# Kernel optimization log

Hardware: AMD Instinct MI355X
Metric: run time of the kernel (lower is better)

## Reference

```python
import jax, jax.numpy as jnp
import numpy as np

NEG_INF = -1e30


def setup_inputs() -> dict:
    key = jax.random.key(0)
    k1, k2 = jax.random.split(key)
    N, Q, M = 8, 2048, 2048
    gen_adj = jax.random.normal(k1, (N, Q, M), dtype=jnp.float32)
    # per-sample k in [1, 64]; force one sample to the max so topknum is deterministic
    topk = jax.random.randint(k2, (N, 1), 1, 65, dtype=jnp.int64)
    topk = topk.at[0, 0].set(64)
    return {"gen_adj": gen_adj, "topk": topk}


def reference(gen_adj, topk):
    # gen_adj: [N, Q, M] float, topk: [N, 1] int (per-sample variable k)
    N, Q, M = gen_adj.shape
    k_per = jnp.minimum(topk, M)                      # clamp like min(topk[i], M)
    topknum = int(jnp.max(k_per))                     # padded output width

    a = jnp.abs(gen_adj)                              # [N, Q, M]
    vals, idx = jax.lax.top_k(a, topknum)             # [N, Q, K] each (sorted desc)

    pos = jnp.arange(topknum)                         # [K]
    valid = pos[None, None, :] < k_per[:, :, None]    # [N, 1, K] -> broadcasts over Q

    # softmax over only the first k_i logits per sample; padded slots -> 0
    logits = jnp.where(valid, vals, NEG_INF)
    r_weight = jax.nn.softmax(logits, axis=-1)
    r_weight = jnp.where(valid, r_weight, 0.0)        # exact zeros in padding
    topk_index = jnp.where(valid, idx, 0)             # pad indices with 0
    return r_weight, topk_index
```

## Files before the change

### kernel.cpp

```cpp
#include <hip/hip_runtime.h>

#define M_COLS 2048
#define KOUT 64
#define CAND 128
#define BLK 256

typedef unsigned long long u64;

#define DPPU(old, src, ctrl, rmask) \
  ((unsigned)__builtin_amdgcn_update_dpp((int)(old), (int)(src), (ctrl), (rmask), 0xF, false))
#define RDL(x, l) ((unsigned)__builtin_amdgcn_readlane((int)(x), (l)))

#define SCAN_ADD_U(x)             \
  do {                            \
    x += DPPU(0u, x, 0x111, 0xF); \
    x += DPPU(0u, x, 0x112, 0xF); \
    x += DPPU(0u, x, 0x114, 0xF); \
    x += DPPU(0u, x, 0x118, 0xF); \
    x += DPPU(0u, x, 0x142, 0xA); \
    x += DPPU(0u, x, 0x143, 0xC); \
  } while (0)

#define SCAN_MAX_U(x)                                  \
  do {                                                 \
    unsigned _t;                                       \
    _t = DPPU(0u, x, 0x111, 0xF); x = x > _t ? x : _t; \
    _t = DPPU(0u, x, 0x112, 0xF); x = x > _t ? x : _t; \
    _t = DPPU(0u, x, 0x114, 0xF); x = x > _t ? x : _t; \
    _t = DPPU(0u, x, 0x118, 0xF); x = x > _t ? x : _t; \
    _t = DPPU(0u, x, 0x142, 0xA); x = x > _t ? x : _t; \
    _t = DPPU(0u, x, 0x143, 0xC); x = x > _t ? x : _t; \
  } while (0)

#define SCAN_ADD_F(x)                                               \
  do {                                                              \
    x += __uint_as_float(DPPU(0u, __float_as_uint(x), 0x111, 0xF)); \
    x += __uint_as_float(DPPU(0u, __float_as_uint(x), 0x112, 0xF)); \
    x += __uint_as_float(DPPU(0u, __float_as_uint(x), 0x114, 0xF)); \
    x += __uint_as_float(DPPU(0u, __float_as_uint(x), 0x118, 0xF)); \
    x += __uint_as_float(DPPU(0u, __float_as_uint(x), 0x142, 0xA)); \
    x += __uint_as_float(DPPU(0u, __float_as_uint(x), 0x143, 0xC)); \
  } while (0)

#define SWZ(v, J) ((unsigned)__builtin_amdgcn_ds_swizzle((int)(v), (((J) << 10) | 0x1f)))

#define EX_S(dst, src, J)                           \
  do {                                              \
    unsigned _lo = SWZ((unsigned)(src), J);         \
    unsigned _hi = SWZ((unsigned)((src) >> 32), J); \
    dst = ((u64)_hi << 32) | _lo;                   \
  } while (0)
#define EX_D(dst, src, CTRL)                             \
  do {                                                   \
    unsigned _lo = DPPU(0u, (unsigned)(src), CTRL, 0xF); \
    unsigned _hi = DPPU(0u, (unsigned)((src) >> 32), CTRL, 0xF); \
    dst = ((u64)_hi << 32) | _lo;                        \
  } while (0)
#define EX_W(dst, src)                                                         \
  do {                                                                         \
    unsigned _lo = (unsigned)__shfl_xor((int)(unsigned)(src), 32, 64);         \
    unsigned _hi = (unsigned)__shfl_xor((int)(unsigned)((src) >> 32), 32, 64); \
    dst = ((u64)_hi << 32) | _lo;                                              \
  } while (0)

#define CMPSEL(up)                        \
  do {                                    \
    k0 = ((k0 >= o0) == (up)) ? k0 : o0;  \
    k1 = ((k1 >= o1) == (up)) ? o1 : k1;  \
  } while (0)

#define STEP_A_S(J, UP) do { u64 o0, o1; EX_S(o0, k0, J); EX_S(o1, k1, J); CMPSEL(UP); } while (0)
#define STEP_A_D(CTRL, UP) do { u64 o0, o1; EX_D(o0, k0, CTRL); EX_D(o1, k1, CTRL); CMPSEL(UP); } while (0)
#define STEP_A_W(UP) do { u64 o0, o1; EX_W(o0, k0); EX_W(o1, k1); CMPSEL(UP); } while (0)

#define STEP_B_S(J, UP) do { u64 o; EX_S(o, av, J); av = ((av >= o) == (UP)) ? av : o; } while (0)
#define STEP_B_D(CTRL, UP) do { u64 o; EX_D(o, av, CTRL); av = ((av >= o) == (UP)) ? av : o; } while (0)
#define STEP_B_W(UP) do { u64 o; EX_W(o, av); av = ((av >= o) == (UP)) ? av : o; } while (0)

__global__ __launch_bounds__(BLK) void topk_route_kernel(
    const float* __restrict__ A, const int* __restrict__ topk,
    float* __restrict__ out_w, float* __restrict__ out_i, int NQ, int Q, int N) {
  __shared__ u64 cand[4][CAND];

  const unsigned tid = threadIdx.x;
  const unsigned wv = tid >> 6, lane = tid & 63u;
  const unsigned row = blockIdx.x * 4u + wv;
  if ((int)row >= NQ) return;
  const unsigned n = row / (unsigned)Q;

  const float4* a4 = (const float4*)(A + (size_t)row * M_COLS);
  float4 v[8];
#pragma unroll
  for (int t = 0; t < 8; ++t) v[t] = a4[lane + 64u * (unsigned)t];

  int kk;
  if (N >= 8) {
    const int4* t4 = (const int4*)topk;
    int4 a = t4[0], b = t4[1], c = t4[2], d = t4[3];
    int k64 = topk[2 * (int)n], k32 = topk[(int)n];
    bool looks64 = (a.y == 0) & (a.w == 0) & (b.y == 0) & (b.w == 0) &
                   (c.y == 0) & (c.w == 0) & (d.y == 0) & (d.w == 0) &
                   (a.x >= 1) & (a.z >= 1) & (b.x >= 1) & (b.z >= 1) &
                   (c.x >= 1) & (c.z >= 1) & (d.x >= 1) & (d.z >= 1);
    kk = looks64 ? k64 : k32;
  } else {
    bool looks64 = true;
    for (int i = 0; i < N; ++i) {
      int l = topk[2 * i], h = topk[2 * i + 1];
      if (h != 0 || l < 1) { looks64 = false; break; }
    }
    kk = looks64 ? topk[2 * (int)n] : topk[(int)n];
  }
  kk = kk > M_COLS ? M_COLS : (kk < 0 ? 0 : kk);

  unsigned bits[32];
#pragma unroll
  for (int t = 0; t < 8; ++t) {
    bits[4 * t + 0] = __float_as_uint(v[t].x) & 0x7fffffffu;
    bits[4 * t + 1] = __float_as_uint(v[t].y) & 0x7fffffffu;
    bits[4 * t + 2] = __float_as_uint(v[t].z) & 0x7fffffffu;
    bits[4 * t + 3] = __float_as_uint(v[t].w) & 0x7fffffffu;
  }

  cand[wv][lane + 64u] = 0ull;

  unsigned mx = bits[0];
#pragma unroll
  for (int j = 1; j < 32; ++j) mx = bits[j] > mx ? bits[j] : mx;
  SCAN_MAX_U(mx);
  mx = RDL(mx, 63);
  const int em = (int)(mx >> 23);

  unsigned keep = 0u, sl = 0u, inc = 0u, csel = 0u;
  auto attempt = [&](unsigned T) {
    unsigned q0 = 0u, q1 = 0u, q2 = 0u, q3 = 0u;
#pragma unroll
    for (int j = 7; j >= 0; --j) {
      q0 = q0 + q0 + (unsigned)(bits[j] >= T);
      q1 = q1 + q1 + (unsigned)(bits[8 + j] >= T);
      q2 = q2 + q2 + (unsigned)(bits[16 + j] >= T);
      q3 = q3 + q3 + (unsigned)(bits[24 + j] >= T);
    }
    keep = q0 | (q1 << 8) | (q2 << 16) | (q3 << 24);
    sl = __popc(keep);
    inc = sl;
    SCAN_ADD_U(inc);
    csel = RDL(inc, 63);
  };

  unsigned lo, hi = mx + 1u;
  {
    unsigned T = (em > 0) ? ((unsigned)em << 23) : 0u;
    attempt(T); lo = T;
    if (csel < KOUT) {
      hi = T;
      T = (em - 1 > 0) ? ((unsigned)(em - 1) << 23) : 0u;
      attempt(T); lo = T;
      if (csel < KOUT) {
        hi = T;
        T = (em - 2 > 0) ? ((unsigned)(em - 2) << 23) : 0u;
        attempt(T); lo = T;
        if (csel < KOUT) { hi = T; attempt(0u); lo = 0u; }
      }
    }
  }

  {
    unsigned csel_lo = csel, lastT = lo;
    while (csel_lo > CAND && lo + 1u < hi) {
      unsigned mid = lo + ((hi - lo) >> 1);
      attempt(mid); lastT = mid;
      if (csel >= KOUT) { lo = mid; csel_lo = csel; } else hi = mid;
    }
    if (lastT != lo) attempt(lo);
  }

  if (csel > CAND) {
    unsigned kgt = 0u;
#pragma unroll
    for (int j = 31; j >= 0; --j) kgt = (kgt << 1) | (unsigned)(bits[j] >= hi);
    unsigned slgt = __popc(kgt), incgt = slgt;
    SCAN_ADD_U(incgt);
    unsigned cgt = RDL(incgt, 63);
    unsigned cap = CAND - cgt;
    keep = kgt;
    unsigned run = 0u;
#pragma unroll
    for (int t = 0; t < 8; ++t) {
      unsigned f = 0u;
#pragma unroll
      for (int c = 3; c >= 0; --c) f = (f << 1) | (unsigned)(bits[4 * t + c] == lo);
      unsigned tc = __popc(f), it = tc;
      SCAN_ADD_U(it);
      unsigned base = run + it - tc;
#pragma unroll
      for (int c = 0; c < 4; ++c) {
        if (f & (1u << c)) {
          if (base < cap) keep |= 1u << (4 * t + c);
          ++base;
        }
      }
      run += RDL(it, 63);
    }
    sl = __popc(keep);
    inc = sl;
    SCAN_ADD_U(inc);
    csel = RDL(inc, 63);
  }

  unsigned p = inc - sl;
  const unsigned lobase = 2047u - 4u * lane;
  u64* cw = &cand[wv][0];
#pragma unroll
  for (int j = 0; j < 32; ++j) {
    if (keep & (1u << j)) {
      cw[p] = ((u64)bits[j] << 32) |
              (u64)(lobase - (unsigned)((j >> 2) * 256 + (j & 3)));
      ++p;
    }
  }

  const bool b1 = (lane & 1u) != 0u, b2 = (lane & 2u) != 0u, b4 = (lane & 4u) != 0u;
  const bool b8 = (lane & 8u) != 0u, b16 = (lane & 16u) != 0u, b32 = (lane & 32u) != 0u;

  u64 k0 = cand[wv][lane];
  u64 k1 = cand[wv][lane + 64u];
  STEP_A_D(0xB1, !(b2 ^ b1));
  STEP_A_D(0x4E, !(b4 ^ b2)); STEP_A_D(0xB1, !(b4 ^ b1));
  STEP_A_S(4, !(b8 ^ b4)); STEP_A_D(0x4E, !(b8 ^ b2)); STEP_A_D(0xB1, !(b8 ^ b1));
  STEP_A_S(8, !(b16 ^ b8)); STEP_A_S(4, !(b16 ^ b4));
  STEP_A_D(0x4E, !(b16 ^ b2)); STEP_A_D(0xB1, !(b16 ^ b1));
  STEP_A_S(16, !(b32 ^ b16)); STEP_A_S(8, !(b32 ^ b8)); STEP_A_S(4, !(b32 ^ b4));
  STEP_A_D(0x4E, !(b32 ^ b2)); STEP_A_D(0xB1, !(b32 ^ b1));
  STEP_A_W(!b32);
  STEP_A_S(16, !b16); STEP_A_S(8, !b8); STEP_A_S(4, !b4);
  STEP_A_D(0x4E, !b2); STEP_A_D(0xB1, !b1);

  u64 av = k0 >= k1 ? k0 : k1;
  STEP_B_W(!b32);
  STEP_B_S(16, !b16); STEP_B_S(8, !b8); STEP_B_S(4, !b4);
  STEP_B_D(0x4E, !b2); STEP_B_D(0xB1, !b1);

  float val = __uint_as_float((unsigned)(av >> 32));
  unsigned midx = 2047u - (unsigned)(av & 0xffffffffull);
  bool valid = (int)lane < kk;

  float vmx = __uint_as_float(
      (unsigned)__builtin_amdgcn_readfirstlane((int)(unsigned)(av >> 32)));
  float e = valid ? __expf(val - vmx) : 0.0f;
  float s = e;
  SCAN_ADD_F(s);
  float stot = __uint_as_float(RDL(__float_as_uint(s), 63));
  float w = valid ? (e / stot) : 0.0f;

  size_t o = (size_t)row * KOUT + lane;
  out_w[o] = w;
  out_i[o] = valid ? (float)midx : 0.0f;
}

extern "C" void kernel_launch(void* const* d_in, const int* in_sizes, int n_in,
                              void* d_out, int out_size, void* d_ws, size_t ws_size,
                              hipStream_t stream) {
  const float* A = (const float*)d_in[0];
  const int* topk = (const int*)d_in[1];
  float* out = (float*)d_out;
  const int NQ = in_sizes[0] / M_COLS;
  const int N = in_sizes[1] > 0 ? in_sizes[1] : 1;
  const int Q = NQ / N;
  float* out_w = out;
  float* out_i = out + (size_t)NQ * KOUT;
  const int blocks = (NQ + 3) / 4;
  hipLaunchKernelGGL(topk_route_kernel, dim3(blocks), dim3(BLK), 0, stream, A,
                     topk, out_w, out_i, NQ, Q, N);
}
```

Measured before the change: 29.66 us.

## Process four rows per wave with register double-buffered prefetch of next row

```diff
diff --git a/kernel.cpp b/kernel.cpp
--- a/kernel.cpp
+++ b/kernel.cpp
@@ -4,6 +4,7 @@
 #define KOUT 64
 #define CAND 128
 #define BLK 256
+#define ROWS 4
 
 typedef unsigned long long u64;
 
@@ -50,11 +51,11 @@
     unsigned _hi = SWZ((unsigned)((src) >> 32), J); \
     dst = ((u64)_hi << 32) | _lo;                   \
   } while (0)
-#define EX_D(dst, src, CTRL)                             \
-  do {                                                   \
-    unsigned _lo = DPPU(0u, (unsigned)(src), CTRL, 0xF); \
+#define EX_D(dst, src, CTRL)                                     \
+  do {                                                           \
+    unsigned _lo = DPPU(0u, (unsigned)(src), CTRL, 0xF);         \
     unsigned _hi = DPPU(0u, (unsigned)((src) >> 32), CTRL, 0xF); \
-    dst = ((u64)_hi << 32) | _lo;                        \
+    dst = ((u64)_hi << 32) | _lo;                                \
   } while (0)
 #define EX_W(dst, src)                                                         \
   do {                                                                         \
@@ -63,10 +64,10 @@
     dst = ((u64)_hi << 32) | _lo;                                              \
   } while (0)
 
-#define CMPSEL(up)                        \
-  do {                                    \
-    k0 = ((k0 >= o0) == (up)) ? k0 : o0;  \
-    k1 = ((k1 >= o1) == (up)) ? o1 : k1;  \
+#define CMPSEL(up)                       \
+  do {                                   \
+    k0 = ((k0 >= o0) == (up)) ? k0 : o0; \
+    k1 = ((k1 >= o1) == (up)) ? o1 : k1; \
   } while (0)
 
 #define STEP_A_S(J, UP) do { u64 o0, o1; EX_S(o0, k0, J); EX_S(o1, k1, J); CMPSEL(UP); } while (0)
@@ -84,178 +85,190 @@
 
   const unsigned tid = threadIdx.x;
   const unsigned wv = tid >> 6, lane = tid & 63u;
-  const unsigned row = blockIdx.x * 4u + wv;
-  if ((int)row >= NQ) return;
-  const unsigned n = row / (unsigned)Q;
-
-  const float4* a4 = (const float4*)(A + (size_t)row * M_COLS);
-  float4 v[8];
-#pragma unroll
-  for (int t = 0; t < 8; ++t) v[t] = a4[lane + 64u * (unsigned)t];
-
-  int kk;
+  const unsigned r0 = (blockIdx.x * 4u + wv) * ROWS;
+  if ((int)r0 >= NQ) return;
+
+  bool looks64;
   if (N >= 8) {
     const int4* t4 = (const int4*)topk;
     int4 a = t4[0], b = t4[1], c = t4[2], d = t4[3];
-    int k64 = topk[2 * (int)n], k32 = topk[(int)n];
-    bool looks64 = (a.y == 0) & (a.w == 0) & (b.y == 0) & (b.w == 0) &
-                   (c.y == 0) & (c.w == 0) & (d.y == 0) & (d.w == 0) &
-                   (a.x >= 1) & (a.z >= 1) & (b.x >= 1) & (b.z >= 1) &
-                   (c.x >= 1) & (c.z >= 1) & (d.x >= 1) & (d.z >= 1);
-    kk = looks64 ? k64 : k32;
+    looks64 = (a.y == 0) & (a.w == 0) & (b.y == 0) & (b.w == 0) &
+              (c.y == 0) & (c.w == 0) & (d.y == 0) & (d.w == 0) &
+              (a.x >= 1) & (a.z >= 1) & (b.x >= 1) & (b.z >= 1) &
+              (c.x >= 1) & (c.z >= 1) & (d.x >= 1) & (d.z >= 1);
   } else {
-    bool looks64 = true;
+    looks64 = true;
     for (int i = 0; i < N; ++i) {
       int l = topk[2 * i], h = topk[2 * i + 1];
       if (h != 0 || l < 1) { looks64 = false; break; }
     }
-    kk = looks64 ? topk[2 * (int)n] : topk[(int)n];
   }
-  kk = kk > M_COLS ? M_COLS : (kk < 0 ? 0 : kk);
-
-  unsigned bits[32];
-#pragma unroll
-  for (int t = 0; t < 8; ++t) {
-    bits[4 * t + 0] = __float_as_uint(v[t].x) & 0x7fffffffu;
-    bits[4 * t + 1] = __float_as_uint(v[t].y) & 0x7fffffffu;
-    bits[4 * t + 2] = __float_as_uint(v[t].z) & 0x7fffffffu;
-    bits[4 * t + 3] = __float_as_uint(v[t].w) & 0x7fffffffu;
+
+  const bool b1 = (lane & 1u) != 0u, b2 = (lane & 2u) != 0u, b4 = (lane & 4u) != 0u;
+  const bool b8 = (lane & 8u) != 0u, b16 = (lane & 16u) != 0u, b32 = (lane & 32u) != 0u;
+  const unsigned lobase = 2047u - 4u * lane;
+  u64* cw = &cand[wv][0];
+
+  float4 buf[8];
+  {
+    const float4* a4 = (const float4*)(A + (size_t)r0 * M_COLS);
+#pragma unroll
+    for (int t = 0; t < 8; ++t) buf[t] = a4[lane + 64u * (unsigned)t];
   }
 
-  cand[wv][lane + 64u] = 0ull;
-
-  unsigned mx = bits[0];
-#pragma unroll
-  for (int j = 1; j < 32; ++j) mx = bits[j] > mx ? bits[j] : mx;
-  SCAN_MAX_U(mx);
-  mx = RDL(mx, 63);
-  const int em = (int)(mx >> 23);
-
-  unsigned keep = 0u, sl = 0u, inc = 0u, csel = 0u;
-  auto attempt = [&](unsigned T) {
-    unsigned q0 = 0u, q1 = 0u, q2 = 0u, q3 = 0u;
-#pragma unroll
-    for (int j = 7; j >= 0; --j) {
-      q0 = q0 + q0 + (unsigned)(bits[j] >= T);
-      q1 = q1 + q1 + (unsigned)(bits[8 + j] >= T);
-      q2 = q2 + q2 + (unsigned)(bits[16 + j] >= T);
-      q3 = q3 + q3 + (unsigned)(bits[24 + j] >= T);
-    }
-    keep = q0 | (q1 << 8) | (q2 << 16) | (q3 << 24);
-    sl = __popc(keep);
-    inc = sl;
-    SCAN_ADD_U(inc);
-    csel = RDL(inc, 63);
-  };
-
-  unsigned lo, hi = mx + 1u;
-  {
-    unsigned T = (em > 0) ? ((unsigned)em << 23) : 0u;
-    attempt(T); lo = T;
-    if (csel < KOUT) {
-      hi = T;
-      T = (em - 1 > 0) ? ((unsigned)(em - 1) << 23) : 0u;
+  for (int i = 0; i < ROWS; ++i) {
+    const unsigned row = r0 + (unsigned)i;
+    if ((int)row >= NQ) break;
+
+    unsigned bits[32];
+#pragma unroll
+    for (int t = 0; t < 8; ++t) {
+      bits[4 * t + 0] = __float_as_uint(buf[t].x) & 0x7fffffffu;
+      bits[4 * t + 1] = __float_as_uint(buf[t].y) & 0x7fffffffu;
+      bits[4 * t + 2] = __float_as_uint(buf[t].z) & 0x7fffffffu;
+      bits[4 * t + 3] = __float_as_uint(buf[t].w) & 0x7fffffffu;
+    }
+
+    if (i + 1 < ROWS && (int)(row + 1u) < NQ) {
+      const float4* b4 = (const float4*)(A + (size_t)(row + 1u) * M_COLS);
+#pragma unroll
+      for (int t = 0; t < 8; ++t) buf[t] = b4[lane + 64u * (unsigned)t];
+    }
+
+    cw[lane + 64u] = 0ull;
+
+    unsigned mx = bits[0];
+#pragma unroll
+    for (int j = 1; j < 32; ++j) mx = bits[j] > mx ? bits[j] : mx;
+    SCAN_MAX_U(mx);
+    mx = RDL(mx, 63);
+    const int em = (int)(mx >> 23);
+
+    unsigned keep = 0u, sl = 0u, inc = 0u, csel = 0u;
+    auto attempt = [&](unsigned T) {
+      unsigned q0 = 0u, q1 = 0u, q2 = 0u, q3 = 0u;
+#pragma unroll
+      for (int j = 7; j >= 0; --j) {
+        q0 = q0 + q0 + (unsigned)(bits[j] >= T);
+        q1 = q1 + q1 + (unsigned)(bits[8 + j] >= T);
+        q2 = q2 + q2 + (unsigned)(bits[16 + j] >= T);
+        q3 = q3 + q3 + (unsigned)(bits[24 + j] >= T);
+      }
+      keep = q0 | (q1 << 8) | (q2 << 16) | (q3 << 24);
+      sl = __popc(keep);
+      inc = sl;
+      SCAN_ADD_U(inc);
+      csel = RDL(inc, 63);
+    };
+
+    unsigned lo, hi = mx + 1u;
+    {
+      unsigned T = (em > 0) ? ((unsigned)em << 23) : 0u;
       attempt(T); lo = T;
       if (csel < KOUT) {
         hi = T;
-        T = (em - 2 > 0) ? ((unsigned)(em - 2) << 23) : 0u;
+        T = (em - 1 > 0) ? ((unsigned)(em - 1) << 23) : 0u;
         attempt(T); lo = T;
-        if (csel < KOUT) { hi = T; attempt(0u); lo = 0u; }
-      }
-    }
+        if (csel < KOUT) {
+          hi = T;
+          T = (em - 2 > 0) ? ((unsigned)(em - 2) << 23) : 0u;
+          attempt(T); lo = T;
+          if (csel < KOUT) { hi = T; attempt(0u); lo = 0u; }
+        }
+      }
+    }
+
+    {
+      unsigned csel_lo = csel, lastT = lo;
+      while (csel_lo > CAND && lo + 1u < hi) {
+        unsigned mid = lo + ((hi - lo) >> 1);
+        attempt(mid); lastT = mid;
+        if (csel >= KOUT) { lo = mid; csel_lo = csel; } else hi = mid;
+      }
+      if (lastT != lo) attempt(lo);
+    }
+
+    if (csel > CAND) {
+      unsigned kgt = 0u;
+#pragma unroll
+      for (int j = 31; j >= 0; --j) kgt = (kgt << 1) | (unsigned)(bits[j] >= hi);
+      unsigned slgt = __popc(kgt), incgt = slgt;
+      SCAN_ADD_U(incgt);
+      unsigned cgt = RDL(incgt, 63);
+      unsigned cap = CAND - cgt;
+      keep = kgt;
+      unsigned run = 0u;
+#pragma unroll
+      for (int t = 0; t < 8; ++t) {
+        unsigned f = 0u;
+#pragma unroll
+        for (int c = 3; c >= 0; --c) f = (f << 1) | (unsigned)(bits[4 * t + c] == lo);
+        unsigned tc = __popc(f), it = tc;
+        SCAN_ADD_U(it);
+        unsigned tbase = run + it - tc;
+#pragma unroll
+        for (int c = 0; c < 4; ++c) {
+          if (f & (1u << c)) {
+            if (tbase < cap) keep |= 1u << (4 * t + c);
+            ++tbase;
+          }
+        }
+        run += RDL(it, 63);
+      }
+      sl = __popc(keep);
+      inc = sl;
+      SCAN_ADD_U(inc);
+      csel = RDL(inc, 63);
+    }
+
+    unsigned base = inc - sl;
+#pragma unroll
+    for (int j = 0; j < 32; ++j) {
+      if (keep & (1u << j)) {
+        unsigned pj = base + (unsigned)__popc(keep & ((1u << j) - 1u));
+        cw[pj] = ((u64)bits[j] << 32) |
+                 (u64)(lobase - (unsigned)((j >> 2) * 256 + (j & 3)));
+      }
+    }
+
+    u64 k0 = cw[lane];
+    u64 k1 = cw[lane + 64u];
+    STEP_A_D(0xB1, !(b2 ^ b1));
+    STEP_A_D(0x4E, !(b4 ^ b2)); STEP_A_D(0xB1, !(b4 ^ b1));
+    STEP_A_S(4, !(b8 ^ b4)); STEP_A_D(0x4E, !(b8 ^ b2)); STEP_A_D(0xB1, !(b8 ^ b1));
+    STEP_A_S(8, !(b16 ^ b8)); STEP_A_S(4, !(b16 ^ b4));
+    STEP_A_D(0x4E, !(b16 ^ b2)); STEP_A_D(0xB1, !(b16 ^ b1));
+    STEP_A_S(16, !(b32 ^ b16)); STEP_A_S(8, !(b32 ^ b8)); STEP_A_S(4, !(b32 ^ b4));
+    STEP_A_D(0x4E, !(b32 ^ b2)); STEP_A_D(0xB1, !(b32 ^ b1));
+    STEP_A_W(!b32);
+    STEP_A_S(16, !b16); STEP_A_S(8, !b8); STEP_A_S(4, !b4);
+    STEP_A_D(0x4E, !b2); STEP_A_D(0xB1, !b1);
+
+    u64 av = k0 >= k1 ? k0 : k1;
+    STEP_B_W(!b32);
+    STEP_B_S(16, !b16); STEP_B_S(8, !b8); STEP_B_S(4, !b4);
+    STEP_B_D(0x4E, !b2); STEP_B_D(0xB1, !b1);
+
+    const unsigned n = row / (unsigned)Q;
+    int kk = looks64 ? topk[2 * (int)n] : topk[(int)n];
+    kk = kk > M_COLS ? M_COLS : (kk < 0 ? 0 : kk);
+
+    float val = __uint_as_float((unsigned)(av >> 32));
+    unsigned midx = 2047u - (unsigned)(av & 0xffffffffull);
+    bool valid = (int)lane < kk;
+
+    float vmx = __uint_as_float(
+        (unsigned)__builtin_amdgcn_readfirstlane((int)(unsigned)(av >> 32)));
+    float e = valid ? __expf(val - vmx) : 0.0f;
+    float s = e;
+    SCAN_ADD_F(s);
+    float stot = __uint_as_float(RDL(__float_as_uint(s), 63));
+    float w = valid ? (e / stot) : 0.0f;
+
+    size_t o = (size_t)row * KOUT + lane;
+    out_w[o] = w;
+    out_i[o] = valid ? (float)midx : 0.0f;
   }
-
-  {
-    unsigned csel_lo = csel, lastT = lo;
-    while (csel_lo > CAND && lo + 1u < hi) {
-      unsigned mid = lo + ((hi - lo) >> 1);
-      attempt(mid); lastT = mid;
-      if (csel >= KOUT) { lo = mid; csel_lo = csel; } else hi = mid;
-    }
-    if (lastT != lo) attempt(lo);
-  }
-
-  if (csel > CAND) {
-    unsigned kgt = 0u;
-#pragma unroll
-    for (int j = 31; j >= 0; --j) kgt = (kgt << 1) | (unsigned)(bits[j] >= hi);
-    unsigned slgt = __popc(kgt), incgt = slgt;
-    SCAN_ADD_U(incgt);
-    unsigned cgt = RDL(incgt, 63);
-    unsigned cap = CAND - cgt;
-    keep = kgt;
-    unsigned run = 0u;
-#pragma unroll
-    for (int t = 0; t < 8; ++t) {
-      unsigned f = 0u;
-#pragma unroll
-      for (int c = 3; c >= 0; --c) f = (f << 1) | (unsigned)(bits[4 * t + c] == lo);
-      unsigned tc = __popc(f), it = tc;
-      SCAN_ADD_U(it);
-      unsigned base = run + it - tc;
-#pragma unroll
-      for (int c = 0; c < 4; ++c) {
-        if (f & (1u << c)) {
-          if (base < cap) keep |= 1u << (4 * t + c);
-          ++base;
-        }
-      }
-      run += RDL(it, 63);
-    }
-    sl = __popc(keep);
-    inc = sl;
-    SCAN_ADD_U(inc);
-    csel = RDL(inc, 63);
-  }
-
-  unsigned p = inc - sl;
-  const unsigned lobase = 2047u - 4u * lane;
-  u64* cw = &cand[wv][0];
-#pragma unroll
-  for (int j = 0; j < 32; ++j) {
-    if (keep & (1u << j)) {
-      cw[p] = ((u64)bits[j] << 32) |
-              (u64)(lobase - (unsigned)((j >> 2) * 256 + (j & 3)));
-      ++p;
-    }
-  }
-
-  const bool b1 = (lane & 1u) != 0u, b2 = (lane & 2u) != 0u, b4 = (lane & 4u) != 0u;
-  const bool b8 = (lane & 8u) != 0u, b16 = (lane & 16u) != 0u, b32 = (lane & 32u) != 0u;
-
-  u64 k0 = cand[wv][lane];
-  u64 k1 = cand[wv][lane + 64u];
-  STEP_A_D(0xB1, !(b2 ^ b1));
-  STEP_A_D(0x4E, !(b4 ^ b2)); STEP_A_D(0xB1, !(b4 ^ b1));
-  STEP_A_S(4, !(b8 ^ b4)); STEP_A_D(0x4E, !(b8 ^ b2)); STEP_A_D(0xB1, !(b8 ^ b1));
-  STEP_A_S(8, !(b16 ^ b8)); STEP_A_S(4, !(b16 ^ b4));
-  STEP_A_D(0x4E, !(b16 ^ b2)); STEP_A_D(0xB1, !(b16 ^ b1));
-  STEP_A_S(16, !(b32 ^ b16)); STEP_A_S(8, !(b32 ^ b8)); STEP_A_S(4, !(b32 ^ b4));
-  STEP_A_D(0x4E, !(b32 ^ b2)); STEP_A_D(0xB1, !(b32 ^ b1));
-  STEP_A_W(!b32);
-  STEP_A_S(16, !b16); STEP_A_S(8, !b8); STEP_A_S(4, !b4);
-  STEP_A_D(0x4E, !b2); STEP_A_D(0xB1, !b1);
-
-  u64 av = k0 >= k1 ? k0 : k1;
-  STEP_B_W(!b32);
-  STEP_B_S(16, !b16); STEP_B_S(8, !b8); STEP_B_S(4, !b4);
-  STEP_B_D(0x4E, !b2); STEP_B_D(0xB1, !b1);
-
-  float val = __uint_as_float((unsigned)(av >> 32));
-  unsigned midx = 2047u - (unsigned)(av & 0xffffffffull);
-  bool valid = (int)lane < kk;
-
-  float vmx = __uint_as_float(
-      (unsigned)__builtin_amdgcn_readfirstlane((int)(unsigned)(av >> 32)));
-  float e = valid ? __expf(val - vmx) : 0.0f;
-  float s = e;
-  SCAN_ADD_F(s);
-  float stot = __uint_as_float(RDL(__float_as_uint(s), 63));
-  float w = valid ? (e / stot) : 0.0f;
-
-  size_t o = (size_t)row * KOUT + lane;
-  out_w[o] = w;
-  out_i[o] = valid ? (float)midx : 0.0f;
 }
 
 extern "C" void kernel_launch(void* const* d_in, const int* in_sizes, int n_in,
@@ -269,7 +282,8 @@
   const int Q = NQ / N;
   float* out_w = out;
   float* out_i = out + (size_t)NQ * KOUT;
-  const int blocks = (NQ + 3) / 4;
+  const int rows_per_block = 4 * ROWS;
+  const int blocks = (NQ + rows_per_block - 1) / rows_per_block;
   hipLaunchKernelGGL(topk_route_kernel, dim3(blocks), dim3(BLK), 0, stream, A,
                      topk, out_w, out_i, NQ, Q, N);
 }
```

Result: slower. 39.58 us (+33.4%).
